# Performance work log

Measured on AMD Instinct MI355X. Metric: run time of the kernel, lower is better.

The kernel has to match this reference:

```python
import jax, jax.numpy as jnp
import numpy as np

N_NODES = 50000
N_EDGES = 1_600_000
IN_DIM = 128
HID = 64


def gcn_conv(x, src, dst, w, W, b, n):
    # PyG GCNConv(normalize=True, add_self_loops=True):
    # add self loops with weight 1, sym-normalize, x@W (no bias in lin), scatter-add, +bias
    loop = jnp.arange(n)
    s = jnp.concatenate([src, loop])
    d = jnp.concatenate([dst, loop])
    ww = jnp.concatenate([w, jnp.ones((n,), w.dtype)])
    deg = jax.ops.segment_sum(ww, d, num_segments=n)                 # [n]
    dis = jnp.where(deg > 0, jax.lax.rsqrt(deg), 0.0)                # deg^{-1/2}, inf->0
    norm = dis[s] * ww * dis[d]                                      # [E+n]
    h = x @ W                                                        # [n, out]
    msg = h[s] * norm[:, None]                                       # gather + scale
    out = jax.ops.segment_sum(msg, d, num_segments=n)                # scatter-add at dst
    return out + b


def setup_inputs() -> dict:
    key = jax.random.key(0)
    ks = jax.random.split(key, 9)
    X = jax.random.normal(ks[0], (N_NODES, IN_DIM), dtype=jnp.float32)
    edge_index = jax.random.randint(ks[1], (2, N_EDGES), 0, N_NODES, dtype=jnp.int64)
    edge_weight = jax.random.uniform(ks[2], (N_EDGES,), dtype=jnp.float32)
    s1 = 1.0 / np.sqrt(IN_DIM)
    s2 = 1.0 / np.sqrt(HID)
    W1 = jax.random.uniform(ks[3], (IN_DIM, HID), jnp.float32, -s1, s1)
    b1 = jax.random.uniform(ks[4], (HID,), jnp.float32, -s1, s1)
    W2 = jax.random.uniform(ks[5], (HID, HID), jnp.float32, -s2, s2)
    b2 = jax.random.uniform(ks[6], (HID,), jnp.float32, -s2, s2)
    Wl = jax.random.uniform(ks[7], (HID, 1), jnp.float32, -s2, s2)
    bl = jax.random.uniform(ks[8], (1,), jnp.float32, -s2, s2)
    return {"X": X, "edge_index": edge_index, "edge_weight": edge_weight,
            "W1": W1, "b1": b1, "W2": W2, "b2": b2, "Wl": Wl, "bl": bl}


def reference(X, edge_index, edge_weight, W1, b1, W2, b2, Wl, bl):
    n = X.shape[0]
    src, dst = edge_index[0], edge_index[1]
    h = jax.nn.relu(gcn_conv(X, src, dst, edge_weight, W1, b1, n))
    # F.dropout(p=0.2) is identity in eval mode
    h = jax.nn.relu(gcn_conv(h, src, dst, edge_weight, W2, b2, n))
    return jax.nn.sigmoid(h @ Wl + bl).squeeze(1)   # [n]
```

## Files before the change

### kernel.cpp

```cpp
#include <hip/hip_runtime.h>

typedef float f32x2 __attribute__((ext_vector_type(2)));

#define A2B 512
#define A2T 512
#define STG 3200

__device__ __forceinline__ long ld_idx(const void* idx, long pos, int is64) {
  return is64 ? (long)((const long long*)idx)[pos]
              : (long)((const int*)idx)[pos];
}

__device__ __forceinline__ int detect_is64(const void* idx) {
  const unsigned long long* p = (const unsigned long long*)idx;
  unsigned long long v = p[threadIdx.x & 63];
  return (__ballot((v >> 32) != 0ull) == 0ull) ? 1 : 0;
}

__device__ __forceinline__ int swz_group(int bid, int GP) {
  int r = bid & 7, q = bid >> 3;
  int j = q / GP;
  int i = q - j * GP;
  return (r + 8 * j) * GP + i;
}

__device__ __forceinline__ uint4 pack16_fp8(const float* acc) {
  uint4 o;
  unsigned v;
  v = 0;
  v = __builtin_amdgcn_cvt_pk_fp8_f32(acc[0],  acc[1],  v, false);
  v = __builtin_amdgcn_cvt_pk_fp8_f32(acc[2],  acc[3],  v, true);
  o.x = v; v = 0;
  v = __builtin_amdgcn_cvt_pk_fp8_f32(acc[4],  acc[5],  v, false);
  v = __builtin_amdgcn_cvt_pk_fp8_f32(acc[6],  acc[7],  v, true);
  o.y = v; v = 0;
  v = __builtin_amdgcn_cvt_pk_fp8_f32(acc[8],  acc[9],  v, false);
  v = __builtin_amdgcn_cvt_pk_fp8_f32(acc[10], acc[11], v, true);
  o.z = v; v = 0;
  v = __builtin_amdgcn_cvt_pk_fp8_f32(acc[12], acc[13], v, false);
  v = __builtin_amdgcn_cvt_pk_fp8_f32(acc[14], acc[15], v, true);
  o.w = v;
  return o;
}

__global__ __launch_bounds__(256) void k_front(const void* __restrict__ idx,
                                               unsigned* __restrict__ histT,
                                               long E, int chunk, unsigned M,
                                               const float* __restrict__ X,
                                               const float* __restrict__ W1,
                                               unsigned char* __restrict__ h, int n) {
  __shared__ float smem[2048];
  const int t = threadIdx.x;
  if (blockIdx.x < A2B) {
    unsigned* cnt = (unsigned*)smem;
    const int b = blockIdx.x;
    const int is64 = detect_is64(idx);
    cnt[t] = 0;
    __syncthreads();
    const long e0 = (long)b * chunk;
    long e1 = e0 + chunk; if (e1 > E) e1 = E;
    for (long e = e0 + t; e < e1; e += 256) {
      unsigned d = (unsigned)ld_idx(idx, E + e, is64);
      atomicAdd(&cnt[__umulhi(d, M)], 1u);
    }
    __syncthreads();
    histT[(size_t)t * A2B + b] = cnt[t];
    return;
  }
  float* Ws = smem;
  for (int i = t; i < 2048; i += 256)
    ((float4*)Ws)[i] = ((const float4*)W1)[i];
  __syncthreads();
  int gid = (blockIdx.x - A2B) * 256 + t;
  int node = gid >> 2;
  int fg = (gid & 3) * 16;
  if (node >= n) return;
  const float4* xr4 = (const float4*)(X + (size_t)node * 128);
  float acc[16];
#pragma unroll
  for (int f = 0; f < 16; ++f) acc[f] = 0.0f;
  for (int k4 = 0; k4 < 32; ++k4) {
    float4 x = xr4[k4];
#pragma unroll
    for (int kk = 0; kk < 4; ++kk) {
      float xv = (kk == 0) ? x.x : (kk == 1) ? x.y : (kk == 2) ? x.z : x.w;
      const float4* wrow = (const float4*)(Ws + (k4 * 4 + kk) * 64 + fg);
#pragma unroll
      for (int f4 = 0; f4 < 4; ++f4) {
        float4 w = wrow[f4];
        acc[f4 * 4 + 0] = fmaf(xv, w.x, acc[f4 * 4 + 0]);
        acc[f4 * 4 + 1] = fmaf(xv, w.y, acc[f4 * 4 + 1]);
        acc[f4 * 4 + 2] = fmaf(xv, w.z, acc[f4 * 4 + 2]);
        acc[f4 * 4 + 3] = fmaf(xv, w.w, acc[f4 * 4 + 3]);
      }
    }
  }
  *(uint4*)(h + (size_t)node * 64 + fg) = pack16_fp8(acc);
}

__global__ __launch_bounds__(256) void k_colscan(const unsigned* __restrict__ histT,
                                                 unsigned* __restrict__ baseT,
                                                 unsigned* __restrict__ colsum) {
  __shared__ unsigned sh[256];
  const int k = blockIdx.x, t = threadIdx.x;
  const uint2 v = ((const uint2*)(histT + (size_t)k * A2B))[t];
  unsigned s = v.x + v.y;
  sh[t] = s;
  __syncthreads();
  for (int off = 1; off < 256; off <<= 1) {
    unsigned u = (t >= off) ? sh[t - off] : 0;
    __syncthreads();
    sh[t] += u;
    __syncthreads();
  }
  unsigned excl = sh[t] - s;
  uint2 o; o.x = excl; o.y = excl + v.x;
  ((uint2*)(baseT + (size_t)k * A2B))[t] = o;
  if (t == 255) colsum[k] = sh[255];
}

__global__ __launch_bounds__(A2T) void k_bucket(const void* __restrict__ idx,
                                                const float* __restrict__ w,
                                                const unsigned* __restrict__ baseT,
                                                const unsigned* __restrict__ colsum,
                                                uint2* __restrict__ recs,
                                                long E, int chunk, unsigned M) {
  __shared__ uint2 stage[STG];
  __shared__ unsigned cnt[256], lofs[256], lbase[256], bcol[256], scanb[256];
  const int b = blockIdx.x, t = threadIdx.x;
  const long e0 = (long)b * chunk;
  long e1 = e0 + chunk; if (e1 > E) e1 = E;
  const int m = (int)(e1 - e0);
  const int is64 = detect_is64(idx);
  if (t < 256) scanb[t] = colsum[t];
  __syncthreads();
  for (int off = 1; off < 256; off <<= 1) {
    unsigned u = 0;
    if (t < 256 && t >= off) u = scanb[t - off];
    __syncthreads();
    if (t < 256) scanb[t] += u;
    __syncthreads();
  }
  if (t < 256) {
    bcol[t] = (scanb[t] - colsum[t]) + baseT[(size_t)t * A2B + b];
    cnt[t] = 0;
  }
  __syncthreads();
  unsigned short dc[8]; unsigned char kc[8];
  int nk = 0;
  for (long e = e0 + t; e < e1; e += A2T, ++nk) {
    unsigned d = (unsigned)ld_idx(idx, E + e, is64);
    unsigned kb = __umulhi(d, M);
    dc[nk] = (unsigned short)d; kc[nk] = (unsigned char)kb;
    atomicAdd(&cnt[kb], 1u);
  }
  __syncthreads();
  if (t < 256) scanb[t] = cnt[t];
  __syncthreads();
  for (int off = 1; off < 256; off <<= 1) {
    unsigned u = 0;
    if (t < 256 && t >= off) u = scanb[t - off];
    __syncthreads();
    if (t < 256) scanb[t] += u;
    __syncthreads();
  }
  if (t < 256) { unsigned ex = scanb[t] - cnt[t]; lbase[t] = ex; lofs[t] = ex; }
  __syncthreads();
  nk = 0;
  for (long e = e0 + t; e < e1; e += A2T, ++nk) {
    unsigned s = (unsigned)ld_idx(idx, e, is64);
    float wv = w[e];
    unsigned kb = kc[nk];
    unsigned pos = atomicAdd(&lofs[kb], 1u);
    stage[pos] = make_uint2(s | ((unsigned)dc[nk] << 16), __float_as_uint(wv));
  }
  __syncthreads();
  for (int i = t; i < m; i += A2T) {
    uint2 r = stage[i];
    unsigned kb = __umulhi(r.x >> 16, M);
    recs[bcol[kb] + (unsigned)i - lbase[kb]] = r;
  }
}

__global__ __launch_bounds__(1024) void k_build(const uint2* __restrict__ recs,
                                                const unsigned* __restrict__ colsum,
                                                int* __restrict__ rowptr,
                                                float* __restrict__ dis,
                                                int n, int dwidth, long E) {
  __shared__ float wsum[256];
  __shared__ unsigned cnt[256], scanb[256];
  __shared__ int shr0, shr1;
  const int k = blockIdx.x, t = threadIdx.x;
  const int d0 = k * dwidth;
  if (t < 256) scanb[t] = colsum[t];
  __syncthreads();
  for (int off = 1; off < 256; off <<= 1) {
    unsigned u = 0;
    if (t < 256 && t >= off) u = scanb[t - off];
    __syncthreads();
    if (t < 256) scanb[t] += u;
    __syncthreads();
  }
  if (t == k) { shr1 = (int)scanb[t]; shr0 = (int)(scanb[t] - colsum[t]); }
  if (t < 256) { wsum[t] = 0.0f; cnt[t] = 0; }
  __syncthreads();
  const int r0 = shr0, r1 = shr1;
  const int m = r1 - r0;
  for (int i = t; i < m; i += 1024) {
    uint2 r = recs[r0 + i];
    int dl = (int)(r.x >> 16) - d0;
    atomicAdd(&cnt[dl], 1u);
    atomicAdd(&wsum[dl], __uint_as_float(r.y));
  }
  __syncthreads();
  if (t < 256) scanb[t] = cnt[t];
  __syncthreads();
  for (int off = 1; off < 256; off <<= 1) {
    unsigned u = 0;
    if (t < 256 && t >= off) u = scanb[t - off];
    __syncthreads();
    if (t < 256) scanb[t] += u;
    __syncthreads();
  }
  if (t < 256) {
    unsigned ex = scanb[t] - cnt[t];
    int d = d0 + t;
    if (t < dwidth && d < n) {
      rowptr[d] = r0 + (int)ex;
      dis[d] = rsqrtf(1.0f + wsum[t]);
    }
  }
  if (k == gridDim.x - 1 && t == 0) rowptr[n] = (int)E;
}

__global__ __launch_bounds__(1024) void k_place(const uint2* __restrict__ recs,
                                                const unsigned* __restrict__ colsum,
                                                const int* __restrict__ rowptr,
                                                const float* __restrict__ dis,
                                                float2* __restrict__ edges,
                                                int n, int dwidth) {
  __shared__ unsigned lofs[256], scanb[256];
  __shared__ int shr0, shr1;
  const int k = blockIdx.x, t = threadIdx.x;
  const int d0 = k * dwidth;
  if (t < 256) scanb[t] = colsum[t];
  __syncthreads();
  for (int off = 1; off < 256; off <<= 1) {
    unsigned u = 0;
    if (t < 256 && t >= off) u = scanb[t - off];
    __syncthreads();
    if (t < 256) scanb[t] += u;
    __syncthreads();
  }
  if (t == k) { shr1 = (int)scanb[t]; shr0 = (int)(scanb[t] - colsum[t]); }
  if (t < 256) {
    int d = d0 + t;
    lofs[t] = (t < dwidth && d < n) ? (unsigned)rowptr[d] : 0u;
  }
  __syncthreads();
  const int r0 = shr0, r1 = shr1;
  const int m = r1 - r0;
  for (int i = t; i < m; i += 1024) {
    uint2 r = recs[r0 + i];
    unsigned src = r.x & 0xffffu;
    float wn = __uint_as_float(r.y) * dis[src];
    unsigned pos = atomicAdd(&lofs[(int)(r.x >> 16) - d0], 1u);
    edges[pos] = make_float2(__uint_as_float(src), wn);
  }
}

__device__ __forceinline__ void gather_acc(const unsigned char* __restrict__ h,
                                           const float2* __restrict__ edges,
                                           int beg, int end, int eg, int fl,
                                           float* acc) {
  f32x2 a0 = {0.0f, 0.0f}, a1 = {0.0f, 0.0f}, a2 = {0.0f, 0.0f}, a3 = {0.0f, 0.0f};
  const unsigned char* hf = h + fl * 8;
  for (int base = beg; base < end; base += 48) {
    float2 rv[12];
#pragma unroll
    for (int s = 0; s < 12; ++s) {
      int idx = base + s * 4 + eg;
      rv[s] = edges[min(idx, end - 1)];
    }
    uint2 hv[12];
#pragma unroll
    for (int s = 0; s < 12; ++s)
      hv[s] = *(const uint2*)(hf + (size_t)__float_as_int(rv[s].x) * 64);
#pragma unroll
    for (int s = 0; s < 12; ++s) {
      float w = (base + s * 4 + eg < end) ? rv[s].y : 0.0f;
      f32x2 nj2 = {w, w};
      a0 += __builtin_amdgcn_cvt_pk_f32_fp8(hv[s].x, false) * nj2;
      a1 += __builtin_amdgcn_cvt_pk_f32_fp8(hv[s].x, true)  * nj2;
      a2 += __builtin_amdgcn_cvt_pk_f32_fp8(hv[s].y, false) * nj2;
      a3 += __builtin_amdgcn_cvt_pk_f32_fp8(hv[s].y, true)  * nj2;
    }
  }
  acc[0] = a0[0]; acc[1] = a0[1]; acc[2] = a1[0]; acc[3] = a1[1];
  acc[4] = a2[0]; acc[5] = a2[1]; acc[6] = a3[0]; acc[7] = a3[1];
#pragma unroll
  for (int off = 8; off < 32; off <<= 1)
#pragma unroll
    for (int i = 0; i < 8; ++i) acc[i] += __shfl_xor(acc[i], off);
}

__device__ __forceinline__ void add_bias_self(const unsigned char* __restrict__ h,
                                              const float* __restrict__ b,
                                              int node, int fl, float s0, float* acc) {
  uint2 hv = *(const uint2*)(h + (size_t)node * 64 + fl * 8);
  f32x2 q0 = __builtin_amdgcn_cvt_pk_f32_fp8(hv.x, false);
  f32x2 q1 = __builtin_amdgcn_cvt_pk_f32_fp8(hv.x, true);
  f32x2 q2 = __builtin_amdgcn_cvt_pk_f32_fp8(hv.y, false);
  f32x2 q3 = __builtin_amdgcn_cvt_pk_f32_fp8(hv.y, true);
  float hs[8] = {q0[0], q0[1], q1[0], q1[1], q2[0], q2[1], q3[0], q3[1]};
  float4 bv0 = *(const float4*)(b + fl * 8);
  float4 bv1 = *(const float4*)(b + fl * 8 + 4);
  float bb[8] = {bv0.x, bv0.y, bv0.z, bv0.w, bv1.x, bv1.y, bv1.z, bv1.w};
  float s2 = s0 * s0;
#pragma unroll
  for (int i = 0; i < 8; ++i) acc[i] += bb[i] + hs[i] * s2;
}

__global__ __launch_bounds__(256) void k_gather_mid(const unsigned char* __restrict__ h,
                                                    const float* __restrict__ dis,
                                                    const float2* __restrict__ edges,
                                                    const int* __restrict__ rowptr,
                                                    const float* __restrict__ b1,
                                                    const float* __restrict__ W2,
                                                    unsigned char* __restrict__ h2,
                                                    int n, int GP) {
  __shared__ float W2s[64 * 64];
  __shared__ float xs[8 * 64];
  const int t = threadIdx.x;
  for (int i = t; i < 1024; i += 256)
    ((float4*)W2s)[i] = ((const float4*)W2)[i];
  int lane = t & 63;
  int l32 = lane & 31;
  int fl = lane & 7;
  int eg = (lane >> 3) & 3;
  int nl = t >> 5;
  const int g = swz_group(blockIdx.x, GP);
  int node = g * 8 + nl;
  int beg = 0, end = 0; float s0 = 0.0f;
  if (node < n) { beg = rowptr[node]; end = rowptr[node + 1]; s0 = dis[node]; }
  float acc[8];
  gather_acc(h, edges, beg, end, eg, fl, acc);
  if (node < n) {
#pragma unroll
    for (int i = 0; i < 8; ++i) acc[i] *= s0;
    add_bias_self(h, b1, node, fl, s0, acc);
    if (eg == 0) {
#pragma unroll
      for (int i = 0; i < 8; ++i) xs[nl * 64 + fl * 8 + i] = fmaxf(acc[i], 0.0f);
    }
  }
  __syncthreads();
  int tl = l32;
  int node2 = g * 8 + (t >> 5);
  if (node2 >= n) return;
  const float* xrow = xs + (t >> 5) * 64;
  int f = tl * 2;
  float a0 = 0.0f, a1 = 0.0f;
#pragma unroll 8
  for (int k = 0; k < 64; ++k) {
    float xk = xrow[k];
    f32x2 wv = *(const f32x2*)(W2s + k * 64 + f);
    a0 = fmaf(xk, wv[0], a0);
    a1 = fmaf(xk, wv[1], a1);
  }
  unsigned v = __builtin_amdgcn_cvt_pk_fp8_f32(a0, a1, 0u, false);
  *(unsigned short*)(h2 + (size_t)node2 * 64 + f) = (unsigned short)v;
}

__global__ __launch_bounds__(256) void k_gather_fin(const unsigned char* __restrict__ h,
                                                    const float* __restrict__ dis,
                                                    const float2* __restrict__ edges,
                                                    const int* __restrict__ rowptr,
                                                    const float* __restrict__ b2,
                                                    const float* __restrict__ Wl,
                                                    const float* __restrict__ bl,
                                                    float* __restrict__ out,
                                                    int n, int GP) {
  int lane = threadIdx.x & 63;
  int l32 = lane & 31;
  int fl = lane & 7;
  int eg = (lane >> 3) & 3;
  const int g = swz_group(blockIdx.x, GP);
  int node = g * 8 + (int)(threadIdx.x >> 5);
  if (node >= n) return;
  int beg = rowptr[node], end = rowptr[node + 1];
  float s0 = dis[node];
  float acc[8];
  gather_acc(h, edges, beg, end, eg, fl, acc);
#pragma unroll
  for (int i = 0; i < 8; ++i) acc[i] *= s0;
  add_bias_self(h, b2, node, fl, s0, acc);
  float4 wl0 = *(const float4*)(Wl + fl * 8);
  float4 wl1 = *(const float4*)(Wl + fl * 8 + 4);
  float wl[8] = {wl0.x, wl0.y, wl0.z, wl0.w, wl1.x, wl1.y, wl1.z, wl1.w};
  float v = 0.0f;
#pragma unroll
  for (int i = 0; i < 8; ++i) v += fmaxf(acc[i], 0.0f) * wl[i];
#pragma unroll
  for (int off = 1; off < 8; off <<= 1) v += __shfl_xor(v, off);
  if (l32 == 0) out[node] = 1.0f / (1.0f + expf(-(v + bl[0])));
}

extern "C" void kernel_launch(void* const* d_in, const int* in_sizes, int n_in,
                              void* d_out, int out_size, void* d_ws, size_t ws_size,
                              hipStream_t stream) {
  const float* X  = (const float*)d_in[0];
  const void*  EI = d_in[1];
  const float* EW = (const float*)d_in[2];
  const float* W1 = (const float*)d_in[3];
  const float* b1 = (const float*)d_in[4];
  const float* W2 = (const float*)d_in[5];
  const float* b2 = (const float*)d_in[6];
  const float* Wl = (const float*)d_in[7];
  const float* bl = (const float*)d_in[8];
  float* out = (float*)d_out;

  const int  n = in_sizes[0] / 128;
  const long E = (long)in_sizes[1] / 2;

  const int chunk  = (int)((E + A2B - 1) / A2B);
  const int dwidth = (((n + 255) / 256) + 7) & ~7;
  const int GP     = dwidth >> 3;
  const unsigned M = (unsigned)((0x100000000ULL + (unsigned)dwidth - 1) / (unsigned)dwidth);

  auto align = [](size_t x) { return (x + 255) & ~(size_t)255; };
  char* ws = (char*)d_ws;
  size_t off = 0;
  float*         dis    = (float*)(ws + off);         off += align((size_t)n * 4);
  int*           rowptr = (int*)(ws + off);           off += align((size_t)(n + 1) * 4);
  unsigned*      colsum = (unsigned*)(ws + off);      off += align(256 * 4);
  unsigned*      histT  = (unsigned*)(ws + off);      off += align((size_t)A2B * 256 * 4);
  unsigned*      baseT  = (unsigned*)(ws + off);      off += align((size_t)A2B * 256 * 4);
  uint2*         recs   = (uint2*)(ws + off);         off += align((size_t)E * 8);
  float2*        edges  = (float2*)(ws + off);        off += align((size_t)E * 8);
  unsigned char* A      = (unsigned char*)(ws + off); off += align((size_t)n * 64);
  unsigned char* A2     = (unsigned char*)(ws + off); off += align((size_t)n * 64);

  const int nbW = 32 * dwidth;
  const int nbG = (n * 4 + 255) / 256;

  k_front<<<A2B + nbG, dim3(256), 0, stream>>>(EI, histT, E, chunk, M, X, W1, A, n);
  k_colscan<<<256, 256, 0, stream>>>(histT, baseT, colsum);
  k_bucket<<<A2B, A2T, 0, stream>>>(EI, EW, baseT, colsum, recs, E, chunk, M);
  k_build<<<256, 1024, 0, stream>>>(recs, colsum, rowptr, dis, n, dwidth, E);
  k_place<<<256, 1024, 0, stream>>>(recs, colsum, rowptr, dis, edges, n, dwidth);

  k_gather_mid<<<nbW, dim3(256), 0, stream>>>(A, dis, edges, rowptr, b1, W2, A2, n, GP);
  k_gather_fin<<<nbW, dim3(256), 0, stream>>>(A2, dis, edges, rowptr, b2, Wl, bl, out, n, GP);
}
```

Baseline: 208.2 us.

## Merge build and place kernels, defer source normalization into gather, move X@W1 into bucket

Measured after the change: 209.6 us. About the same (+0.7%).

```diff
diff --git a/kernel.cpp b/kernel.cpp
--- a/kernel.cpp
+++ b/kernel.cpp
@@ -45,57 +45,21 @@
 
 __global__ __launch_bounds__(256) void k_front(const void* __restrict__ idx,
                                                unsigned* __restrict__ histT,
-                                               long E, int chunk, unsigned M,
-                                               const float* __restrict__ X,
-                                               const float* __restrict__ W1,
-                                               unsigned char* __restrict__ h, int n) {
-  __shared__ float smem[2048];
+                                               long E, int chunk, unsigned M) {
+  __shared__ unsigned cnt[256];
   const int t = threadIdx.x;
-  if (blockIdx.x < A2B) {
-    unsigned* cnt = (unsigned*)smem;
-    const int b = blockIdx.x;
-    const int is64 = detect_is64(idx);
-    cnt[t] = 0;
-    __syncthreads();
-    const long e0 = (long)b * chunk;
-    long e1 = e0 + chunk; if (e1 > E) e1 = E;
-    for (long e = e0 + t; e < e1; e += 256) {
-      unsigned d = (unsigned)ld_idx(idx, E + e, is64);
-      atomicAdd(&cnt[__umulhi(d, M)], 1u);
-    }
-    __syncthreads();
-    histT[(size_t)t * A2B + b] = cnt[t];
-    return;
-  }
-  float* Ws = smem;
-  for (int i = t; i < 2048; i += 256)
-    ((float4*)Ws)[i] = ((const float4*)W1)[i];
-  __syncthreads();
-  int gid = (blockIdx.x - A2B) * 256 + t;
-  int node = gid >> 2;
-  int fg = (gid & 3) * 16;
-  if (node >= n) return;
-  const float4* xr4 = (const float4*)(X + (size_t)node * 128);
-  float acc[16];
-#pragma unroll
-  for (int f = 0; f < 16; ++f) acc[f] = 0.0f;
-  for (int k4 = 0; k4 < 32; ++k4) {
-    float4 x = xr4[k4];
-#pragma unroll
-    for (int kk = 0; kk < 4; ++kk) {
-      float xv = (kk == 0) ? x.x : (kk == 1) ? x.y : (kk == 2) ? x.z : x.w;
-      const float4* wrow = (const float4*)(Ws + (k4 * 4 + kk) * 64 + fg);
-#pragma unroll
-      for (int f4 = 0; f4 < 4; ++f4) {
-        float4 w = wrow[f4];
-        acc[f4 * 4 + 0] = fmaf(xv, w.x, acc[f4 * 4 + 0]);
-        acc[f4 * 4 + 1] = fmaf(xv, w.y, acc[f4 * 4 + 1]);
-        acc[f4 * 4 + 2] = fmaf(xv, w.z, acc[f4 * 4 + 2]);
-        acc[f4 * 4 + 3] = fmaf(xv, w.w, acc[f4 * 4 + 3]);
-      }
-    }
-  }
-  *(uint4*)(h + (size_t)node * 64 + fg) = pack16_fp8(acc);
+  const int b = blockIdx.x;
+  const int is64 = detect_is64(idx);
+  cnt[t] = 0;
+  __syncthreads();
+  const long e0 = (long)b * chunk;
+  long e1 = e0 + chunk; if (e1 > E) e1 = E;
+  for (long e = e0 + t; e < e1; e += 256) {
+    unsigned d = (unsigned)ld_idx(idx, E + e, is64);
+    atomicAdd(&cnt[__umulhi(d, M)], 1u);
+  }
+  __syncthreads();
+  histT[(size_t)t * A2B + b] = cnt[t];
 }
 
 __global__ __launch_bounds__(256) void k_colscan(const unsigned* __restrict__ histT,
@@ -124,10 +88,46 @@
                                                 const unsigned* __restrict__ baseT,
                                                 const unsigned* __restrict__ colsum,
                                                 uint2* __restrict__ recs,
-                                                long E, int chunk, unsigned M) {
-  __shared__ uint2 stage[STG];
+                                                long E, int chunk, unsigned M,
+                                                const float* __restrict__ X,
+                                                const float* __restrict__ W1,
+                                                unsigned char* __restrict__ h, int n) {
+  __shared__ uint2 stage[4096];
   __shared__ unsigned cnt[256], lofs[256], lbase[256], bcol[256], scanb[256];
-  const int b = blockIdx.x, t = threadIdx.x;
+  const int t = threadIdx.x;
+  if (blockIdx.x >= A2B) {
+    float* Ws = (float*)stage;
+    for (int i = t; i < 2048; i += A2T)
+      ((float4*)Ws)[i] = ((const float4*)W1)[i];
+    __syncthreads();
+    int gid = (blockIdx.x - A2B) * A2T + t;
+    int node = gid >> 2;
+    int fg = (gid & 3) * 16;
+    if (node >= n) return;
+    const float4* xr4 = (const float4*)(X + (size_t)node * 128);
+    float acc[16];
+#pragma unroll
+    for (int f = 0; f < 16; ++f) acc[f] = 0.0f;
+    for (int k4 = 0; k4 < 32; ++k4) {
+      float4 x = xr4[k4];
+#pragma unroll
+      for (int kk = 0; kk < 4; ++kk) {
+        float xv = (kk == 0) ? x.x : (kk == 1) ? x.y : (kk == 2) ? x.z : x.w;
+        const float4* wrow = (const float4*)(Ws + (k4 * 4 + kk) * 64 + fg);
+#pragma unroll
+        for (int f4 = 0; f4 < 4; ++f4) {
+          float4 wv = wrow[f4];
+          acc[f4 * 4 + 0] = fmaf(xv, wv.x, acc[f4 * 4 + 0]);
+          acc[f4 * 4 + 1] = fmaf(xv, wv.y, acc[f4 * 4 + 1]);
+          acc[f4 * 4 + 2] = fmaf(xv, wv.z, acc[f4 * 4 + 2]);
+          acc[f4 * 4 + 3] = fmaf(xv, wv.w, acc[f4 * 4 + 3]);
+        }
+      }
+    }
+    *(uint4*)(h + (size_t)node * 64 + fg) = pack16_fp8(acc);
+    return;
+  }
+  const int b = blockIdx.x;
   const long e0 = (long)b * chunk;
   long e1 = e0 + chunk; if (e1 > E) e1 = E;
   const int m = (int)(e1 - e0);
@@ -182,13 +182,14 @@
   }
 }
 
-__global__ __launch_bounds__(1024) void k_build(const uint2* __restrict__ recs,
-                                                const unsigned* __restrict__ colsum,
-                                                int* __restrict__ rowptr,
-                                                float* __restrict__ dis,
-                                                int n, int dwidth, long E) {
+__global__ __launch_bounds__(1024) void k_bp(const uint2* __restrict__ recs,
+                                             const unsigned* __restrict__ colsum,
+                                             int* __restrict__ rowptr,
+                                             float* __restrict__ dis,
+                                             float2* __restrict__ edges,
+                                             int n, int dwidth, long E) {
   __shared__ float wsum[256];
-  __shared__ unsigned cnt[256], scanb[256];
+  __shared__ unsigned cnt[256], lofs[256], scanb[256];
   __shared__ int shr0, shr1;
   const int k = blockIdx.x, t = threadIdx.x;
   const int d0 = k * dwidth;
@@ -224,6 +225,7 @@
   }
   if (t < 256) {
     unsigned ex = scanb[t] - cnt[t];
+    lofs[t] = (unsigned)r0 + ex;
     int d = d0 + t;
     if (t < dwidth && d < n) {
       rowptr[d] = r0 + (int)ex;
@@ -231,45 +233,16 @@
     }
   }
   if (k == gridDim.x - 1 && t == 0) rowptr[n] = (int)E;
-}
-
-__global__ __launch_bounds__(1024) void k_place(const uint2* __restrict__ recs,
-                                                const unsigned* __restrict__ colsum,
-                                                const int* __restrict__ rowptr,
-                                                const float* __restrict__ dis,
-                                                float2* __restrict__ edges,
-                                                int n, int dwidth) {
-  __shared__ unsigned lofs[256], scanb[256];
-  __shared__ int shr0, shr1;
-  const int k = blockIdx.x, t = threadIdx.x;
-  const int d0 = k * dwidth;
-  if (t < 256) scanb[t] = colsum[t];
-  __syncthreads();
-  for (int off = 1; off < 256; off <<= 1) {
-    unsigned u = 0;
-    if (t < 256 && t >= off) u = scanb[t - off];
-    __syncthreads();
-    if (t < 256) scanb[t] += u;
-    __syncthreads();
-  }
-  if (t == k) { shr1 = (int)scanb[t]; shr0 = (int)(scanb[t] - colsum[t]); }
-  if (t < 256) {
-    int d = d0 + t;
-    lofs[t] = (t < dwidth && d < n) ? (unsigned)rowptr[d] : 0u;
-  }
-  __syncthreads();
-  const int r0 = shr0, r1 = shr1;
-  const int m = r1 - r0;
+  __syncthreads();
   for (int i = t; i < m; i += 1024) {
     uint2 r = recs[r0 + i];
-    unsigned src = r.x & 0xffffu;
-    float wn = __uint_as_float(r.y) * dis[src];
     unsigned pos = atomicAdd(&lofs[(int)(r.x >> 16) - d0], 1u);
-    edges[pos] = make_float2(__uint_as_float(src), wn);
+    edges[pos] = make_float2(__uint_as_float(r.x & 0xffffu), __uint_as_float(r.y));
   }
 }
 
 __device__ __forceinline__ void gather_acc(const unsigned char* __restrict__ h,
+                                           const float* __restrict__ dis,
                                            const float2* __restrict__ edges,
                                            int beg, int end, int eg, int fl,
                                            float* acc) {
@@ -282,13 +255,20 @@
       int idx = base + s * 4 + eg;
       rv[s] = edges[min(idx, end - 1)];
     }
+    int sj[12];
+    float nj[12];
+#pragma unroll
+    for (int s = 0; s < 12; ++s) {
+      sj[s] = __float_as_int(rv[s].x);
+      nj[s] = rv[s].y * dis[sj[s]];
+    }
     uint2 hv[12];
 #pragma unroll
     for (int s = 0; s < 12; ++s)
-      hv[s] = *(const uint2*)(hf + (size_t)__float_as_int(rv[s].x) * 64);
+      hv[s] = *(const uint2*)(hf + (size_t)sj[s] * 64);
 #pragma unroll
     for (int s = 0; s < 12; ++s) {
-      float w = (base + s * 4 + eg < end) ? rv[s].y : 0.0f;
+      float w = (base + s * 4 + eg < end) ? nj[s] : 0.0f;
       f32x2 nj2 = {w, w};
       a0 += __builtin_amdgcn_cvt_pk_f32_fp8(hv[s].x, false) * nj2;
       a1 += __builtin_amdgcn_cvt_pk_f32_fp8(hv[s].x, true)  * nj2;
@@ -344,7 +324,7 @@
   int beg = 0, end = 0; float s0 = 0.0f;
   if (node < n) { beg = rowptr[node]; end = rowptr[node + 1]; s0 = dis[node]; }
   float acc[8];
-  gather_acc(h, edges, beg, end, eg, fl, acc);
+  gather_acc(h, dis, edges, beg, end, eg, fl, acc);
   if (node < n) {
 #pragma unroll
     for (int i = 0; i < 8; ++i) acc[i] *= s0;
@@ -391,7 +371,7 @@
   int beg = rowptr[node], end = rowptr[node + 1];
   float s0 = dis[node];
   float acc[8];
-  gather_acc(h, edges, beg, end, eg, fl, acc);
+  gather_acc(h, dis, edges, beg, end, eg, fl, acc);
 #pragma unroll
   for (int i = 0; i < 8; ++i) acc[i] *= s0;
   add_bias_self(h, b2, node, fl, s0, acc);
@@ -441,14 +421,14 @@
   unsigned char* A      = (unsigned char*)(ws + off); off += align((size_t)n * 64);
   unsigned char* A2     = (unsigned char*)(ws + off); off += align((size_t)n * 64);
 
-  const int nbW = 32 * dwidth;
-  const int nbG = (n * 4 + 255) / 256;
-
-  k_front<<<A2B + nbG, dim3(256), 0, stream>>>(EI, histT, E, chunk, M, X, W1, A, n);
+  const int nbW  = 32 * dwidth;
+  const int nbG  = (n * 4 + A2T - 1) / A2T;
+
+  k_front<<<A2B, dim3(256), 0, stream>>>(EI, histT, E, chunk, M);
   k_colscan<<<256, 256, 0, stream>>>(histT, baseT, colsum);
-  k_bucket<<<A2B, A2T, 0, stream>>>(EI, EW, baseT, colsum, recs, E, chunk, M);
-  k_build<<<256, 1024, 0, stream>>>(recs, colsum, rowptr, dis, n, dwidth, E);
-  k_place<<<256, 1024, 0, stream>>>(recs, colsum, rowptr, dis, edges, n, dwidth);
+  k_bucket<<<A2B + nbG, dim3(A2T), 0, stream>>>(EI, EW, baseT, colsum, recs, E, chunk, M,
+                                                X, W1, A, n);
+  k_bp<<<256, dim3(1024), 0, stream>>>(recs, colsum, rowptr, dis, edges, n, dwidth, E);
 
   k_gather_mid<<<nbW, dim3(256), 0, stream>>>(A, dis, edges, rowptr, b1, W2, A2, n, GP);
   k_gather_fin<<<nbW, dim3(256), 0, stream>>>(A2, dis, edges, rowptr, b2, Wl, bl, out, n, GP);
```
